# Performance work log

Hardware: AMD Instinct MI355X
Metric: run time of the kernel (lower is better)

The kernel has to match this reference:

```python
import jax, jax.numpy as jnp
import numpy as np

D_MODEL = 1024
N_HEAD = 16
SEQ = 2048
BATCH = 2


def setup_inputs() -> dict:
    key = jax.random.key(0)
    x = jax.random.normal(key, (BATCH, SEQ, D_MODEL), dtype=jnp.float32)
    return {"x": x}


def reference(x) -> jnp.ndarray:
    B, S, D = x.shape
    H = N_HEAD
    hd = D // H
    # split heads: q=k=v=x -> [B, H, S, hd]
    qkv = x.reshape(B, S, H, hd).transpose(0, 2, 1, 3)
    q = k = v = qkv
    # scores [B, H, S, S], scaled by sqrt(head_dim)
    w = jnp.einsum("bhqd,bhkd->bhqk", q, k) / jnp.sqrt(jnp.asarray(hd, x.dtype))
    # causal mask (nd == ns == S here)
    causal = jnp.tril(jnp.ones((S, S), dtype=bool))
    mask_value = jnp.finfo(w.dtype).min
    w = jnp.where(causal[None, None, :, :], w, mask_value)
    w = jax.nn.softmax(w, axis=-1)
    out = jnp.einsum("bhqk,bhkd->bhqd", w, v)
    # merge heads -> [B, S, D]
    return out.transpose(0, 2, 1, 3).reshape(B, S, D)
```

## Files before the change

### kernel.cpp

```cpp
#include <hip/hip_runtime.h>
#include <hip/hip_bf16.h>

#define BATCH  2
#define SEQ    2048
#define DMODEL 1024
#define NHEAD  16
#define HD     64
#define BH     (BATCH * NHEAD)

typedef __attribute__((ext_vector_type(8))) short s8v;
typedef __attribute__((ext_vector_type(16))) float f16v;
typedef __attribute__((ext_vector_type(4))) unsigned u4v;

#define QK_BETA 0.42466089f

__device__ inline unsigned short bf16_rne(float f) {
    unsigned u = __builtin_bit_cast(unsigned, f);
    u += 0x7FFFu + ((u >> 16) & 1u);
    return (unsigned short)(u >> 16);
}

__device__ __forceinline__ unsigned pk_bf16(float lo, float hi) {
    __hip_bfloat162 h = __float22bfloat162_rn(make_float2(lo, hi));
    unsigned u;
    __builtin_memcpy(&u, &h, 4);
    return u;
}

__device__ __forceinline__ void pl32swap(unsigned& a, unsigned& b) {
    asm volatile("v_permlane32_swap_b32 %0, %1" : "+v"(a), "+v"(b));
}

__global__ __launch_bounds__(256) void prep_kernel(const float* __restrict__ x,
                                                   unsigned short* __restrict__ xb,
                                                   unsigned short* __restrict__ xbT) {
    __shared__ unsigned short tileT[64 * 40];
    const int id = blockIdx.x;
    const int bh = id & (BH - 1);
    const int st = id >> 5;
    const int b = bh >> 4, h = bh & (NHEAD - 1);
    const int s0 = st * 32;
    const int tid = threadIdx.x;
    const int c4 = tid & 15, r16 = tid >> 4;

    const size_t off0 = (size_t)(b * SEQ + s0 + r16) * DMODEL + h * HD + c4 * 4;
    const size_t off1 = (size_t)(b * SEQ + s0 + 16 + r16) * DMODEL + h * HD + c4 * 4;
    const float4 v0 = *(const float4*)(x + off0);
    const float4 v1 = *(const float4*)(x + off1);

    {
        uint2 u;
        u.x = pk_bf16(v0.x * QK_BETA, v0.y * QK_BETA);
        u.y = pk_bf16(v0.z * QK_BETA, v0.w * QK_BETA);
        *(uint2*)(xb + off0) = u;
        u.x = pk_bf16(v1.x * QK_BETA, v1.y * QK_BETA);
        u.y = pk_bf16(v1.z * QK_BETA, v1.w * QK_BETA);
        *(uint2*)(xb + off1) = u;
    }
    {
        const int d0 = c4 * 4;
        unsigned short* t0 = tileT + r16;
        t0[(d0 + 0) * 40] = bf16_rne(v0.x);
        t0[(d0 + 1) * 40] = bf16_rne(v0.y);
        t0[(d0 + 2) * 40] = bf16_rne(v0.z);
        t0[(d0 + 3) * 40] = bf16_rne(v0.w);
        unsigned short* t1 = tileT + 16 + r16;
        t1[(d0 + 0) * 40] = bf16_rne(v1.x);
        t1[(d0 + 1) * 40] = bf16_rne(v1.y);
        t1[(d0 + 2) * 40] = bf16_rne(v1.z);
        t1[(d0 + 3) * 40] = bf16_rne(v1.w);
    }
    __syncthreads();
    {
        const int d = tid >> 2;
        const int sq = (tid & 3) * 8;
        const s8v o = *(const s8v*)(tileT + d * 40 + sq);
        *(s8v*)(xbT + (size_t)(bh * HD + d) * SEQ + s0 + sq) = o;
    }
}

__device__ __forceinline__ void stage_tile2(const unsigned short* __restrict__ xbh,
                                            const unsigned short* __restrict__ xTh,
                                            char* lds, int bufoff, int k0,
                                            int w, int sr, int sc) {
    if (w == 0) {
#pragma unroll
        for (int i = 0; i < 8; ++i) {
            const int r = i * 8 + sr;
            const unsigned short* gsrc =
                xbh + (size_t)(k0 + r) * DMODEL + ((sc ^ (r & 7)) * 8);
            const int loff = __builtin_amdgcn_readfirstlane(bufoff + i * 1024);
            __builtin_amdgcn_global_load_lds(
                (const __attribute__((address_space(1))) void*)gsrc,
                (__attribute__((address_space(3))) void*)(lds + loff), 16, 0, 0);
        }
    } else {
#pragma unroll
        for (int i = 0; i < 8; ++i) {
            const int d = i * 8 + sr;
            const unsigned short* gsrc =
                xTh + (size_t)d * SEQ + k0 + ((sc ^ (d & 7)) * 8);
            const int loff = __builtin_amdgcn_readfirstlane(bufoff + 8192 + i * 1024);
            __builtin_amdgcn_global_load_lds(
                (const __attribute__((address_space(1))) void*)gsrc,
                (__attribute__((address_space(3))) void*)(lds + loff), 16, 0, 0);
        }
    }
}

__global__ __launch_bounds__(128, 2) void flash_kernel(const unsigned short* __restrict__ xb,
                                                       const unsigned short* __restrict__ xbT,
                                                       float* __restrict__ out) {
    __shared__ __align__(16) char lds[32768];

    const int id = blockIdx.x;
    const int bh = id & (BH - 1);
    const int t5 = id >> 5;
    const int rr = t5 >> 3, uu = t5 & 7;
    const int qt = (rr == 0) ? (31 - uu) : (rr == 1) ? (16 + uu)
                 : (rr == 2) ? (15 - uu) : uu;
    const int b = bh >> 4, h = bh & (NHEAD - 1);
    const int tid = threadIdx.x;
    const int w = tid >> 6;
    const int lane = tid & 63;
    const int qh = lane & 31;
    const int hh = lane >> 5;
    const int qbase = qt * 64;

    const unsigned short* xbh = xb + (size_t)b * SEQ * DMODEL + h * HD;
    const unsigned short* xTh = xbT + (size_t)bh * HD * SEQ;

    const int qrow = qbase + w * 32 + qh;
    const s8v qf0 = *(const s8v*)(xbh + (size_t)qrow * DMODEL + 0 * 16 + hh * 8);
    const s8v qf1 = *(const s8v*)(xbh + (size_t)qrow * DMODEL + 1 * 16 + hh * 8);
    const s8v qf2 = *(const s8v*)(xbh + (size_t)qrow * DMODEL + 2 * 16 + hh * 8);
    const s8v qf3 = *(const s8v*)(xbh + (size_t)qrow * DMODEL + 3 * 16 + hh * 8);

    int kbo[2][4], vbo[2][4];
#pragma unroll
    for (int i2 = 0; i2 < 2; ++i2)
#pragma unroll
        for (int c = 0; c < 4; ++c) {
            kbo[i2][c] = (i2 * 32 + qh) * 128 + (((2 * c + hh) ^ (qh & 7)) * 16);
            vbo[i2][c] = 8192 + (i2 * 32 + qh) * 128 + (((2 * c + hh) ^ (qh & 7)) * 16);
        }

    f16v o0 = {0,0,0,0,0,0,0,0,0,0,0,0,0,0,0,0};
    f16v o1 = o0;
    float lsum = 0.0f;

    const int sr = lane >> 3;
    const int sc = lane & 7;

    stage_tile2(xbh, xTh, lds, 0, 0, w, sr, sc);

    for (int kt = 0; kt <= qt; ++kt) {
        char* const buf = lds + ((kt & 1) << 14);
        __syncthreads();
        if (kt < qt)
            stage_tile2(xbh, xTh, lds, ((kt & 1) ^ 1) << 14, (kt + 1) * 64, w, sr, sc);

        const int base_off = qbase + w * 32 - kt * 64;
        const bool fullLive = (base_off >= 63);
        const int qlim = base_off + qh;

        f16v c0 = {0,0,0,0,0,0,0,0,0,0,0,0,0,0,0,0};
        f16v c1 = c0;
        __builtin_amdgcn_s_setprio(1);
        c0 = __builtin_amdgcn_mfma_f32_32x32x16_bf16(*(const s8v*)(buf + kbo[0][0]), qf0, c0, 0, 0, 0);
        c0 = __builtin_amdgcn_mfma_f32_32x32x16_bf16(*(const s8v*)(buf + kbo[0][1]), qf1, c0, 0, 0, 0);
        c0 = __builtin_amdgcn_mfma_f32_32x32x16_bf16(*(const s8v*)(buf + kbo[0][2]), qf2, c0, 0, 0, 0);
        c0 = __builtin_amdgcn_mfma_f32_32x32x16_bf16(*(const s8v*)(buf + kbo[0][3]), qf3, c0, 0, 0, 0);
        c1 = __builtin_amdgcn_mfma_f32_32x32x16_bf16(*(const s8v*)(buf + kbo[1][0]), qf0, c1, 0, 0, 0);
        c1 = __builtin_amdgcn_mfma_f32_32x32x16_bf16(*(const s8v*)(buf + kbo[1][1]), qf1, c1, 0, 0, 0);
        c1 = __builtin_amdgcn_mfma_f32_32x32x16_bf16(*(const s8v*)(buf + kbo[1][2]), qf2, c1, 0, 0, 0);
        c1 = __builtin_amdgcn_mfma_f32_32x32x16_bf16(*(const s8v*)(buf + kbo[1][3]), qf3, c1, 0, 0, 0);
        __builtin_amdgcn_s_setprio(0);

        float p0[16], p1[16];
#pragma unroll
        for (int e = 0; e < 16; ++e) {
            p0[e] = __builtin_amdgcn_exp2f(c0[e]);
            p1[e] = __builtin_amdgcn_exp2f(c1[e]);
        }
        if (!fullLive) {
#pragma unroll
            for (int e = 0; e < 16; ++e) {
                const int kl = (e & 3) + 8 * (e >> 2) + 4 * hh;
                p0[e] = (kl <= qlim) ? p0[e] : 0.0f;
                p1[e] = (kl + 32 <= qlim) ? p1[e] : 0.0f;
            }
        }
#pragma unroll
        for (int e = 0; e < 16; ++e) lsum += p0[e] + p1[e];

        unsigned u0[8], u1[8];
#pragma unroll
        for (int m = 0; m < 8; ++m) {
            u0[m] = pk_bf16(p0[2 * m], p0[2 * m + 1]);
            u1[m] = pk_bf16(p1[2 * m], p1[2 * m + 1]);
        }
        u4v pw0, pw1, pw2, pw3;
        {
            unsigned a, b2;
            a = u0[0]; b2 = u0[2]; pl32swap(a, b2); pw0[0] = a; pw0[2] = b2;
            a = u0[1]; b2 = u0[3]; pl32swap(a, b2); pw0[1] = a; pw0[3] = b2;
            a = u0[4]; b2 = u0[6]; pl32swap(a, b2); pw1[0] = a; pw1[2] = b2;
            a = u0[5]; b2 = u0[7]; pl32swap(a, b2); pw1[1] = a; pw1[3] = b2;
            a = u1[0]; b2 = u1[2]; pl32swap(a, b2); pw2[0] = a; pw2[2] = b2;
            a = u1[1]; b2 = u1[3]; pl32swap(a, b2); pw2[1] = a; pw2[3] = b2;
            a = u1[4]; b2 = u1[6]; pl32swap(a, b2); pw3[0] = a; pw3[2] = b2;
            a = u1[5]; b2 = u1[7]; pl32swap(a, b2); pw3[1] = a; pw3[3] = b2;
        }
        const s8v pa0 = __builtin_bit_cast(s8v, pw0);
        const s8v pa1 = __builtin_bit_cast(s8v, pw1);
        const s8v pa2 = __builtin_bit_cast(s8v, pw2);
        const s8v pa3 = __builtin_bit_cast(s8v, pw3);

        __builtin_amdgcn_s_setprio(1);
        o0 = __builtin_amdgcn_mfma_f32_32x32x16_bf16(pa0, *(const s8v*)(buf + vbo[0][0]), o0, 0, 0, 0);
        o1 = __builtin_amdgcn_mfma_f32_32x32x16_bf16(pa0, *(const s8v*)(buf + vbo[1][0]), o1, 0, 0, 0);
        o0 = __builtin_amdgcn_mfma_f32_32x32x16_bf16(pa1, *(const s8v*)(buf + vbo[0][1]), o0, 0, 0, 0);
        o1 = __builtin_amdgcn_mfma_f32_32x32x16_bf16(pa1, *(const s8v*)(buf + vbo[1][1]), o1, 0, 0, 0);
        o0 = __builtin_amdgcn_mfma_f32_32x32x16_bf16(pa2, *(const s8v*)(buf + vbo[0][2]), o0, 0, 0, 0);
        o1 = __builtin_amdgcn_mfma_f32_32x32x16_bf16(pa2, *(const s8v*)(buf + vbo[1][2]), o1, 0, 0, 0);
        o0 = __builtin_amdgcn_mfma_f32_32x32x16_bf16(pa3, *(const s8v*)(buf + vbo[0][3]), o0, 0, 0, 0);
        o1 = __builtin_amdgcn_mfma_f32_32x32x16_bf16(pa3, *(const s8v*)(buf + vbo[1][3]), o1, 0, 0, 0);
        __builtin_amdgcn_s_setprio(0);
    }

    lsum += __shfl_xor(lsum, 32, 64);
    float invr[16];
#pragma unroll
    for (int e = 0; e < 16; ++e) {
        const int rowq = (e & 3) + 8 * (e >> 2) + 4 * hh;
        invr[e] = 1.0f / __shfl(lsum, rowq, 64);
    }

    float* outh = out + (size_t)b * SEQ * DMODEL + h * HD;
#pragma unroll
    for (int e = 0; e < 16; ++e) {
        const int rowq = (e & 3) + 8 * (e >> 2) + 4 * hh;
        const size_t ro = (size_t)(qbase + w * 32 + rowq) * DMODEL;
        outh[ro + 0 * 32 + qh] = o0[e] * invr[e];
        outh[ro + 1 * 32 + qh] = o1[e] * invr[e];
    }
}

#define KT 32
#define QR 16
#define LDS_STRIDE 68

__global__ __launch_bounds__(64, 2)
void attn_fp32_kernel(const float* __restrict__ x, float* __restrict__ out) {
    __shared__ float kv[KT * LDS_STRIDE];
    const int id = blockIdx.x;
    const int bh = id & (BATCH * NHEAD - 1);
    const int qt = (SEQ / QR - 1) - (id >> 5);
    const int b = bh >> 4, h = bh & (NHEAD - 1);
    const int lane = threadIdx.x;
    const int row = lane & (QR - 1);
    const int slice = lane >> 4;
    const int qrow = qt * QR + row;
    const float* xh = x + (size_t)b * SEQ * DMODEL + (size_t)h * HD;
    float q[HD], o[HD];
    const float4* qp = (const float4*)(xh + (size_t)qrow * DMODEL);
#pragma unroll
    for (int i = 0; i < HD / 4; ++i) {
        float4 v = qp[i];
        q[4*i+0] = v.x * 0.125f; q[4*i+1] = v.y * 0.125f;
        q[4*i+2] = v.z * 0.125f; q[4*i+3] = v.w * 0.125f;
    }
#pragma unroll
    for (int d = 0; d < HD; ++d) o[d] = 0.0f;
    float l = 0.0f;
    const int kend = qt * QR + QR;
    for (int kt0 = 0; kt0 < kend; kt0 += KT) {
        __syncthreads();
#pragma unroll
        for (int i = 0; i < (KT * HD / 4) / 64; ++i) {
            int idx = i * 64 + lane;
            int r = idx >> 4, cc = idx & 15;
            *(float4*)(kv + r * LDS_STRIDE + cc * 4) =
                *(const float4*)(xh + (size_t)(kt0 + r) * DMODEL + cc * 4);
        }
        __syncthreads();
#pragma unroll 2
        for (int jj = 0; jj < KT / 4; ++jj) {
            const int j = jj * 4 + slice;
            const float* kr = kv + j * LDS_STRIDE;
            float a0 = 0.f, a1 = 0.f, a2 = 0.f, a3 = 0.f;
#pragma unroll
            for (int dq = 0; dq < 16; ++dq) {
                float4 kk = ((const float4*)kr)[dq];
                a0 = fmaf(q[4*dq+0], kk.x, a0); a1 = fmaf(q[4*dq+1], kk.y, a1);
                a2 = fmaf(q[4*dq+2], kk.z, a2); a3 = fmaf(q[4*dq+3], kk.w, a3);
            }
            float p = __expf((a0 + a1) + (a2 + a3));
            p = (kt0 + j <= qrow) ? p : 0.0f;
            l += p;
#pragma unroll
            for (int dq = 0; dq < 16; ++dq) {
                float4 vv = ((const float4*)kr)[dq];
                o[4*dq+0] = fmaf(p, vv.x, o[4*dq+0]); o[4*dq+1] = fmaf(p, vv.y, o[4*dq+1]);
                o[4*dq+2] = fmaf(p, vv.z, o[4*dq+2]); o[4*dq+3] = fmaf(p, vv.w, o[4*dq+3]);
            }
        }
    }
    l += __shfl_xor(l, 16, 64);
    l += __shfl_xor(l, 32, 64);
#pragma unroll
    for (int d = 0; d < HD; ++d) {
        o[d] += __shfl_xor(o[d], 16, 64);
        o[d] += __shfl_xor(o[d], 32, 64);
    }
    if (slice == 0) {
        const float invl = 1.0f / l;
        float4* op = (float4*)(out + ((size_t)b * SEQ + qrow) * DMODEL + (size_t)h * HD);
#pragma unroll
        for (int i = 0; i < HD / 4; ++i) {
            float4 v;
            v.x = o[4*i+0] * invl; v.y = o[4*i+1] * invl;
            v.z = o[4*i+2] * invl; v.w = o[4*i+3] * invl;
            op[i] = v;
        }
    }
}

extern "C" void kernel_launch(void* const* d_in, const int* in_sizes, int n_in,
                              void* d_out, int out_size, void* d_ws, size_t ws_size,
                              hipStream_t stream) {
    const float* x = (const float*)d_in[0];
    float* out = (float*)d_out;
    const size_t nXb = (size_t)BATCH * SEQ * DMODEL;
    const size_t need = 2 * nXb * 2;
    if (ws_size >= need) {
        unsigned short* xb  = (unsigned short*)d_ws;
        unsigned short* xbT = xb + nXb;
        hipLaunchKernelGGL(prep_kernel, dim3(BH * SEQ / 32), dim3(256), 0, stream,
                           x, xb, xbT);
        hipLaunchKernelGGL(flash_kernel, dim3(BH * SEQ / 64), dim3(128), 0, stream,
                           xb, xbT, out);
    } else {
        hipLaunchKernelGGL(attn_fp32_kernel, dim3(BATCH * NHEAD * (SEQ / QR)), dim3(64), 0,
                           stream, x, out);
    }
}
```

Before: 104.8 us.

## Software-pipeline QK^T of next tile with softmax and PV of current tile

Restructures the key-tile loop into a two-stage software pipeline. The QK^T MFMAs and the V fragment loads for tile kt+1 are issued before the exp, mask, pack and PV MFMAs of tile kt, and the loop is unrolled by two with ping-pong PipeTile register sets. V is held in registers, so the LDS buffer can be restaged right away. The aim is to overlap MFMA work with the transcendental and packing ALU work inside each wave, since occupancy is low. The cost is much higher register pressure from two live score tiles and sixteen V fragments, which risks spills or lower occupancy.

```diff
diff --git a/kernel.cpp b/kernel.cpp
--- a/kernel.cpp
+++ b/kernel.cpp
@@ -107,6 +107,12 @@
         }
     }
 }
+
+struct PipeTile {
+    f16v c0, c1;
+    s8v v0, v1, v2, v3, v4, v5, v6, v7;
+    int boff;
+};
 
 __global__ __launch_bounds__(128, 2) void flash_kernel(const unsigned short* __restrict__ xb,
                                                        const unsigned short* __restrict__ xbT,
@@ -152,18 +158,9 @@
     const int sr = lane >> 3;
     const int sc = lane & 7;
 
-    stage_tile2(xbh, xTh, lds, 0, 0, w, sr, sc);
-
-    for (int kt = 0; kt <= qt; ++kt) {
-        char* const buf = lds + ((kt & 1) << 14);
-        __syncthreads();
-        if (kt < qt)
-            stage_tile2(xbh, xTh, lds, ((kt & 1) ^ 1) << 14, (kt + 1) * 64, w, sr, sc);
-
-        const int base_off = qbase + w * 32 - kt * 64;
-        const bool fullLive = (base_off >= 63);
-        const int qlim = base_off + qh;
-
+    auto qkload = [&](PipeTile& T, int kt) {
+        const char* buf = lds + ((kt & 1) << 14);
+        T.boff = qbase + w * 32 - kt * 64;
         f16v c0 = {0,0,0,0,0,0,0,0,0,0,0,0,0,0,0,0};
         f16v c1 = c0;
         __builtin_amdgcn_s_setprio(1);
@@ -176,14 +173,26 @@
         c1 = __builtin_amdgcn_mfma_f32_32x32x16_bf16(*(const s8v*)(buf + kbo[1][2]), qf2, c1, 0, 0, 0);
         c1 = __builtin_amdgcn_mfma_f32_32x32x16_bf16(*(const s8v*)(buf + kbo[1][3]), qf3, c1, 0, 0, 0);
         __builtin_amdgcn_s_setprio(0);
-
+        T.c0 = c0; T.c1 = c1;
+        T.v0 = *(const s8v*)(buf + vbo[0][0]);
+        T.v1 = *(const s8v*)(buf + vbo[1][0]);
+        T.v2 = *(const s8v*)(buf + vbo[0][1]);
+        T.v3 = *(const s8v*)(buf + vbo[1][1]);
+        T.v4 = *(const s8v*)(buf + vbo[0][2]);
+        T.v5 = *(const s8v*)(buf + vbo[1][2]);
+        T.v6 = *(const s8v*)(buf + vbo[0][3]);
+        T.v7 = *(const s8v*)(buf + vbo[1][3]);
+    };
+
+    auto finish = [&](const PipeTile& T) {
         float p0[16], p1[16];
 #pragma unroll
         for (int e = 0; e < 16; ++e) {
-            p0[e] = __builtin_amdgcn_exp2f(c0[e]);
-            p1[e] = __builtin_amdgcn_exp2f(c1[e]);
-        }
-        if (!fullLive) {
+            p0[e] = __builtin_amdgcn_exp2f(T.c0[e]);
+            p1[e] = __builtin_amdgcn_exp2f(T.c1[e]);
+        }
+        if (!(T.boff >= 63)) {
+            const int qlim = T.boff + qh;
 #pragma unroll
             for (int e = 0; e < 16; ++e) {
                 const int kl = (e & 3) + 8 * (e >> 2) + 4 * hh;
@@ -218,15 +227,45 @@
         const s8v pa3 = __builtin_bit_cast(s8v, pw3);
 
         __builtin_amdgcn_s_setprio(1);
-        o0 = __builtin_amdgcn_mfma_f32_32x32x16_bf16(pa0, *(const s8v*)(buf + vbo[0][0]), o0, 0, 0, 0);
-        o1 = __builtin_amdgcn_mfma_f32_32x32x16_bf16(pa0, *(const s8v*)(buf + vbo[1][0]), o1, 0, 0, 0);
-        o0 = __builtin_amdgcn_mfma_f32_32x32x16_bf16(pa1, *(const s8v*)(buf + vbo[0][1]), o0, 0, 0, 0);
-        o1 = __builtin_amdgcn_mfma_f32_32x32x16_bf16(pa1, *(const s8v*)(buf + vbo[1][1]), o1, 0, 0, 0);
-        o0 = __builtin_amdgcn_mfma_f32_32x32x16_bf16(pa2, *(const s8v*)(buf + vbo[0][2]), o0, 0, 0, 0);
-        o1 = __builtin_amdgcn_mfma_f32_32x32x16_bf16(pa2, *(const s8v*)(buf + vbo[1][2]), o1, 0, 0, 0);
-        o0 = __builtin_amdgcn_mfma_f32_32x32x16_bf16(pa3, *(const s8v*)(buf + vbo[0][3]), o0, 0, 0, 0);
-        o1 = __builtin_amdgcn_mfma_f32_32x32x16_bf16(pa3, *(const s8v*)(buf + vbo[1][3]), o1, 0, 0, 0);
+        o0 = __builtin_amdgcn_mfma_f32_32x32x16_bf16(pa0, T.v0, o0, 0, 0, 0);
+        o1 = __builtin_amdgcn_mfma_f32_32x32x16_bf16(pa0, T.v1, o1, 0, 0, 0);
+        o0 = __builtin_amdgcn_mfma_f32_32x32x16_bf16(pa1, T.v2, o0, 0, 0, 0);
+        o1 = __builtin_amdgcn_mfma_f32_32x32x16_bf16(pa1, T.v3, o1, 0, 0, 0);
+        o0 = __builtin_amdgcn_mfma_f32_32x32x16_bf16(pa2, T.v4, o0, 0, 0, 0);
+        o1 = __builtin_amdgcn_mfma_f32_32x32x16_bf16(pa2, T.v5, o1, 0, 0, 0);
+        o0 = __builtin_amdgcn_mfma_f32_32x32x16_bf16(pa3, T.v6, o0, 0, 0, 0);
+        o1 = __builtin_amdgcn_mfma_f32_32x32x16_bf16(pa3, T.v7, o1, 0, 0, 0);
         __builtin_amdgcn_s_setprio(0);
+    };
+
+    PipeTile tA, tB;
+
+    stage_tile2(xbh, xTh, lds, 0, 0, w, sr, sc);
+    __syncthreads();
+    if (qt > 0)
+        stage_tile2(xbh, xTh, lds, 1 << 14, 64, w, sr, sc);
+    qkload(tA, 0);
+
+    int kt = 1;
+    for (; kt + 1 <= qt; kt += 2) {
+        __syncthreads();
+        if (kt < qt)
+            stage_tile2(xbh, xTh, lds, ((kt + 1) & 1) << 14, (kt + 1) * 64, w, sr, sc);
+        qkload(tB, kt);
+        finish(tA);
+        __syncthreads();
+        if (kt + 1 < qt)
+            stage_tile2(xbh, xTh, lds, (kt & 1) << 14, (kt + 2) * 64, w, sr, sc);
+        qkload(tA, kt + 1);
+        finish(tB);
+    }
+    if (kt <= qt) {
+        __syncthreads();
+        qkload(tB, kt);
+        finish(tA);
+        finish(tB);
+    } else {
+        finish(tA);
     }
 
     lsum += __shfl_xor(lsum, 32, 64);
```

Result: no change. 105.1 us (+0.2%).
